# Optimization experiments

Measured on AMD Instinct MI355X. Metric: run time of the kernel, lower is better.

The kernel has to match this reference:

```python
import jax, jax.numpy as jnp
import numpy as np


def silu(x):
    return x * jax.nn.sigmoid(x)


def setup_inputs() -> dict:
    key = jax.random.key(0)
    ks = jax.random.split(key, 12)
    B, S, Dm = 2, 2048, 768
    I, N, R, K = 1536, 16, 48, 4
    s = 0.02
    return {
        "input_states": jax.random.normal(ks[0], (B, S, Dm), jnp.float32),
        "in_proj_w": jax.random.normal(ks[1], (2 * I, Dm), jnp.float32) * s,
        "conv_w": jax.random.normal(ks[2], (I, 1, K), jnp.float32) * s,
        "conv_b": jax.random.normal(ks[3], (I,), jnp.float32) * s,
        "x_proj_w": jax.random.normal(ks[4], (R + 2 * N, I), jnp.float32) * s,
        "dt_proj_w": jax.random.normal(ks[5], (I, R), jnp.float32) * s,
        "dt_proj_b": jax.random.normal(ks[6], (I,), jnp.float32) * s,
        "A_log": jax.random.normal(ks[7], (I, N), jnp.float32) * 0.5,
        "D": jax.random.normal(ks[8], (I,), jnp.float32) * s,
        "out_proj_w": jax.random.normal(ks[9], (Dm, I), jnp.float32) * s,
        "alpha": jax.random.uniform(ks[10], (I,), jnp.float32),
        "feature_gating": jax.random.uniform(ks[11], (I,), jnp.float32),
    }


def reference(input_states, in_proj_w, conv_w, conv_b, x_proj_w,
              dt_proj_w, dt_proj_b, A_log, D, out_proj_w,
              alpha, feature_gating):
    Bsz, S, _ = input_states.shape
    I, N = A_log.shape
    R = dt_proj_w.shape[1]
    K = conv_w.shape[-1]

    # in_proj (no bias), chunk into hidden / gate, each [B, I, S]
    proj = jnp.einsum('bsd,ed->bse', input_states, in_proj_w)  # [B, S, 2I]
    hidden, gate = jnp.split(proj.transpose(0, 2, 1), 2, axis=1)

    # causal depthwise conv1d + SiLU
    h = jax.lax.conv_general_dilated(
        hidden, conv_w, window_strides=(1,), padding=[(K - 1, 0)],
        dimension_numbers=('NCH', 'OIH', 'NCH'), feature_group_count=I)
    h = silu(h + conv_b[None, :, None])  # [B, I, S]

    # x_proj -> time_step, B, C
    ssm_p = jnp.einsum('bis,ei->bse', h, x_proj_w)  # [B, S, R+2N]
    ts, Bm, Cm = jnp.split(ssm_p, [R, R + N], axis=-1)

    dt = jax.nn.softplus(jnp.einsum('bsr,ir->bsi', ts, dt_proj_w) + dt_proj_b)
    dt = dt.transpose(0, 2, 1)                       # [B, I, S]
    dt = dt.at[:, :, -1].multiply(alpha[None, :])    # alpha scales last step

    A = -jnp.exp(A_log.astype(jnp.float32))          # [I, N]
    dA = jnp.exp(A[None, :, None, :] * dt[:, :, :, None])       # [B, I, S, N]
    dBu = dt[:, :, :, None] * Bm[:, None, :, :] * h[:, :, :, None]  # [B, I, S, N]

    def step(state, xs):
        dA_t, dBu_t, C_t = xs
        state = dA_t * state + dBu_t                 # [B, I, N]
        y = jnp.einsum('bin,bn->bi', state, C_t)
        return state, y

    init = jnp.zeros((Bsz, I, N), input_states.dtype)
    _, ys = jax.lax.scan(
        step, init,
        (dA.transpose(2, 0, 1, 3), dBu.transpose(2, 0, 1, 3), Cm.transpose(1, 0, 2)))
    y = ys.transpose(1, 2, 0)                        # [B, I, S]

    y = (y + h * D[None, :, None]) * silu(gate)
    y = y.at[:, :, -1].multiply(feature_gating[None, :])
    return jnp.einsum('bis,di->bsd', y, out_proj_w)  # [B, S, Dm]
```

## Files before the change

kernel.cpp:

```cpp
#include <hip/hip_runtime.h>
#include <math.h>


static constexpr int S_LEN  = 2048;
static constexpr int DMODEL = 768;
static constexpr int ICH    = 1536;
static constexpr int NST    = 16;
static constexpr int MROWS  = 4096;
static constexpr int NCH    = 64;
static constexpr int CHS    = 32;
static constexpr int CSTR   = 2 * ICH * NST;

typedef _Float16 f16;
typedef f16 f16x8 __attribute__((ext_vector_type(8)));
typedef f16 f16x4 __attribute__((ext_vector_type(4)));
typedef f16 f16x2 __attribute__((ext_vector_type(2)));
typedef float f32x4 __attribute__((ext_vector_type(4)));

#if __has_builtin(__builtin_amdgcn_exp2f)
#define EXP2F(x) __builtin_amdgcn_exp2f(x)
#else
#define EXP2F(x) exp2f(x)
#endif

typedef __attribute__((address_space(3))) void lds_void;
typedef const __attribute__((address_space(1))) void glb_void;

__device__ __forceinline__ void glds16(f16* l, const f16* g) {
    __builtin_amdgcn_global_load_lds((glb_void*)g, (lds_void*)l, 16, 0, 0);
}

__device__ __forceinline__ float silu_f(float x) {
    return x / (1.0f + __expf(-x));
}

__global__ __launch_bounds__(256) void cvt3(
    const float* __restrict__ s0, f16* __restrict__ d0, int n0,
    const float* __restrict__ s1, f16* __restrict__ d1, int n1,
    const float* __restrict__ s2, f16* __restrict__ d2)
{
    int i = (blockIdx.x * 256 + threadIdx.x) * 4;
    const float* s; f16* d;
    if (i < n0)            { s = s0 + i;            d = d0 + i; }
    else if (i < n0 + n1)  { s = s1 + (i - n0);     d = d1 + (i - n0); }
    else                   { s = s2 + (i - n0 - n1); d = d2 + (i - n0 - n1); }
    float4 v = *(const float4*)s;
    f16x4 o = { (f16)v.x, (f16)v.y, (f16)v.z, (f16)v.w };
    *(f16x4*)d = o;
}

__global__ __launch_bounds__(256) void k1m(
    const f16* __restrict__ Xh,
    const f16* __restrict__ Wh,
    f16* __restrict__ hidden,
    f16* __restrict__ sgate)
{
    __shared__ __align__(16) f16 As[2][128 * 32];
    __shared__ __align__(16) f16 Bs[2][64 * 32];
    const int tid = threadIdx.x;
    const int lane = tid & 63, wave = tid >> 6;
    const int quad = lane >> 4, l16 = lane & 15;
    const int wm = wave & 1, wn = wave >> 1;
    const int m0 = blockIdx.x * 128, n0 = blockIdx.y * 64;
    const int l_row = lane >> 2, l_c8 = (lane & 3) * 8;

    const f16* Ag = Xh + (size_t)(m0 + wave * 16 + l_row) * 768 + l_c8;
    const f16* Bg = Wh + (size_t)(n0 + wave * 16 + l_row) * 768 + l_c8;
    const int aLo = (wave * 16) * 32, aHi = (64 + wave * 16) * 32;
    const int bOff = (wave * 16) * 32;

#define K1_STAGE(buf, kk)                                        \
    do {                                                         \
        glds16(&As[buf][aLo], Ag + (kk));                        \
        glds16(&As[buf][aHi], Ag + (size_t)64 * 768 + (kk));     \
        glds16(&Bs[buf][bOff], Bg + (kk));                       \
    } while (0)

#define K1_COMPUTE(buf)                                                        \
    do {                                                                       \
        f16x8 af[4], bf[2];                                                    \
        _Pragma("unroll")                                                      \
        for (int mi = 0; mi < 4; ++mi)                                         \
            af[mi] = *(const f16x8*)&As[buf][(wm * 64 + mi * 16 + l16) * 32 + quad * 8]; \
        _Pragma("unroll")                                                      \
        for (int ni = 0; ni < 2; ++ni)                                         \
            bf[ni] = *(const f16x8*)&Bs[buf][(wn * 32 + ni * 16 + l16) * 32 + quad * 8]; \
        _Pragma("unroll")                                                      \
        for (int mi = 0; mi < 4; ++mi)                                         \
            _Pragma("unroll")                                                  \
            for (int ni = 0; ni < 2; ++ni)                                     \
                acc[mi][ni] = __builtin_amdgcn_mfma_f32_16x16x32_f16(          \
                    af[mi], bf[ni], acc[mi][ni], 0, 0, 0);                     \
    } while (0)

    K1_STAGE(0, 0);
    __syncthreads();

    f32x4 acc[4][2] = {};
    for (int k0 = 0; k0 < 768; k0 += 64) {
        K1_STAGE(1, k0 + 32);
        K1_COMPUTE(0);
        __syncthreads();
        if (k0 + 64 < 768) K1_STAGE(0, k0 + 64);
        K1_COMPUTE(1);
        __syncthreads();
    }
#undef K1_STAGE
#undef K1_COMPUTE

    const bool isGate = (n0 >= ICH);
    f16* outp = isGate ? sgate : hidden;
    const int e0 = (isGate ? (n0 - ICH) : n0) + wn * 32 + l16;
    #pragma unroll
    for (int mi = 0; mi < 4; ++mi) {
        #pragma unroll
        for (int ni = 0; ni < 2; ++ni) {
            #pragma unroll
            for (int r = 0; r < 4; ++r) {
                int m = m0 + wm * 64 + mi * 16 + quad * 4 + r;
                int e = e0 + ni * 16;
                float v = acc[mi][ni][r];
                if (isGate) v = silu_f(v);
                outp[(size_t)m * ICH + e] = (f16)v;
            }
        }
    }
}

__global__ __launch_bounds__(256) void k3m(
    const f16* __restrict__ hidden,
    const float* __restrict__ conv_w,
    const float* __restrict__ conv_b,
    const float* __restrict__ xw,
    f16* __restrict__ h,
    float* __restrict__ ssmp)
{
    __shared__ __align__(16) f16 Ah[128 * 32];
    __shared__ __align__(16) f16 Bh[80 * 32];
    __shared__ float4 cwv[96];
    __shared__ float  cbv[96];
    const int tid = threadIdx.x;
    const int lane = tid & 63, wave = tid >> 6;
    const int quad = lane >> 4, l16 = lane & 15;
    const int m0 = blockIdx.x * 128;
    const int kbeg = blockIdx.y * 96;

    if (tid < 96) {
        cwv[tid] = *(const float4*)(conv_w + (size_t)(kbeg + tid) * 4);
        cbv[tid] = conv_b[kbeg + tid];
    }

    f32x4 acc[2][5] = {};
    for (int k0 = kbeg; k0 < kbeg + 96; k0 += 32) {
        __syncthreads();
        #pragma unroll
        for (int it = 0; it < 2; ++it) {
            int slot = tid + it * 256;
            int r_ = slot >> 2, c_ = (slot & 3) * 8;
            int gm = m0 + r_, c = k0 + c_;
            int s = gm & (S_LEN - 1);
            const f16* bp = hidden + (size_t)gm * ICH + c;
            f16x8 x0 = *(const f16x8*)bp;
            f16x8 x1 = *(const f16x8*)(bp - (s >= 1 ? ICH : 0));
            f16x8 x2 = *(const f16x8*)(bp - (s >= 2 ? 2 * ICH : 0));
            f16x8 x3 = *(const f16x8*)(bp - (s >= 3 ? 3 * ICH : 0));
            f16x8 o;
            #pragma unroll
            for (int j = 0; j < 8; ++j) {
                int ci = (k0 - kbeg) + c_ + j;
                float4 w = cwv[ci];
                float v1 = (s >= 1) ? (float)x1[j] : 0.f;
                float v2 = (s >= 2) ? (float)x2[j] : 0.f;
                float v3 = (s >= 3) ? (float)x3[j] : 0.f;
                float r = cbv[ci] + w.x * v3 + w.y * v2 + w.z * v1 + w.w * (float)x0[j];
                o[j] = (f16)silu_f(r);
            }
            *(f16x8*)&Ah[r_ * 32 + c_] = o;
            *(f16x8*)(h + (size_t)gm * ICH + c) = o;
        }
        {
            int c4 = (tid & 7) * 4;
            for (int r = tid >> 3; r < 80; r += 32) {
                float4 v = *(const float4*)(xw + (size_t)r * ICH + k0 + c4);
                f16x4 o = { (f16)v.x, (f16)v.y, (f16)v.z, (f16)v.w };
                *(f16x4*)&Bh[r * 32 + c4] = o;
            }
        }
        __syncthreads();
        f16x8 af[2], bf[5];
        #pragma unroll
        for (int mi = 0; mi < 2; ++mi)
            af[mi] = *(const f16x8*)&Ah[(wave * 32 + mi * 16 + l16) * 32 + quad * 8];
        #pragma unroll
        for (int j = 0; j < 5; ++j)
            bf[j] = *(const f16x8*)&Bh[(j * 16 + l16) * 32 + quad * 8];
        #pragma unroll
        for (int mi = 0; mi < 2; ++mi)
            #pragma unroll
            for (int j = 0; j < 5; ++j)
                acc[mi][j] = __builtin_amdgcn_mfma_f32_16x16x32_f16(
                    af[mi], bf[j], acc[mi][j], 0, 0, 0);
    }
    #pragma unroll
    for (int mi = 0; mi < 2; ++mi) {
        #pragma unroll
        for (int j = 0; j < 5; ++j) {
            #pragma unroll
            for (int r = 0; r < 4; ++r) {
                int m = m0 + wave * 32 + mi * 16 + quad * 4 + r;
                atomicAdd(ssmp + (size_t)m * 80 + j * 16 + l16, acc[mi][j][r]);
            }
        }
    }
}

__global__ __launch_bounds__(256) void k4m(
    const float* __restrict__ ssmp,
    const float* __restrict__ dtw,
    const float* __restrict__ dtb,
    const float* __restrict__ alpha,
    f16* __restrict__ dt)
{
    __shared__ __align__(16) f16 As[128 * 72];
    __shared__ __align__(16) f16 Bs[128 * 72];
    const int tid = threadIdx.x;
    const int lane = tid & 63, wave = tid >> 6;
    const int quad = lane >> 4, l16 = lane & 15;
    const int wm = wave & 1, wn = wave >> 1;
    const int m0 = blockIdx.x * 128, n0 = blockIdx.y * 128;
    const int srow = tid >> 1;
    const int shalf = tid & 1;

    {
        const float* sa = ssmp + (size_t)(m0 + srow) * 80 + shalf * 24;
        const float* sb = dtw + (size_t)(n0 + srow) * 48 + shalf * 24;
        f16* da = &As[srow * 72 + shalf * 24];
        f16* db = &Bs[srow * 72 + shalf * 24];
        #pragma unroll
        for (int j = 0; j < 6; ++j) {
            float4 va = *(const float4*)(sa + 4 * j);
            float4 vb = *(const float4*)(sb + 4 * j);
            f16x4 oa = { (f16)va.x, (f16)va.y, (f16)va.z, (f16)va.w };
            f16x4 ob = { (f16)vb.x, (f16)vb.y, (f16)vb.z, (f16)vb.w };
            *(f16x4*)(da + 4 * j) = oa;
            *(f16x4*)(db + 4 * j) = ob;
        }
        if (shalf) {
            f16x8 z = {};
            *(f16x8*)&As[srow * 72 + 48] = z;
            *(f16x8*)&As[srow * 72 + 56] = z;
            *(f16x8*)&Bs[srow * 72 + 48] = z;
            *(f16x8*)&Bs[srow * 72 + 56] = z;
        }
    }
    __syncthreads();

    f32x4 acc[4][4] = {};
    #pragma unroll
    for (int ks = 0; ks < 2; ++ks) {
        f16x8 af[4], bf[4];
        #pragma unroll
        for (int mi = 0; mi < 4; ++mi)
            af[mi] = *(const f16x8*)&As[(wm * 64 + mi * 16 + l16) * 72 + ks * 32 + quad * 8];
        #pragma unroll
        for (int ni = 0; ni < 4; ++ni)
            bf[ni] = *(const f16x8*)&Bs[(wn * 64 + ni * 16 + l16) * 72 + ks * 32 + quad * 8];
        #pragma unroll
        for (int mi = 0; mi < 4; ++mi)
            #pragma unroll
            for (int ni = 0; ni < 4; ++ni)
                acc[mi][ni] = __builtin_amdgcn_mfma_f32_16x16x32_f16(
                    af[mi], bf[ni], acc[mi][ni], 0, 0, 0);
    }

    #pragma unroll
    for (int ni = 0; ni < 4; ++ni) {
        int e = n0 + wn * 64 + ni * 16 + l16;
        float bias = dtb[e];
        float al = alpha[e];
        #pragma unroll
        for (int mi = 0; mi < 4; ++mi) {
            #pragma unroll
            for (int r = 0; r < 4; ++r) {
                int m = m0 + wm * 64 + mi * 16 + quad * 4 + r;
                float x = acc[mi][ni][r] + bias;
                float sp = (x > 20.0f) ? x : __logf(1.0f + __expf(x));
                if ((m & (S_LEN - 1)) == S_LEN - 1) sp *= al;
                dt[(size_t)m * ICH + e] = (f16)sp;
            }
        }
    }
}

__global__ __launch_bounds__(256) void k5a_chunk(
    const f16* __restrict__ dt,
    const f16* __restrict__ h,
    const float* __restrict__ ssmp,
    const float* __restrict__ A_log,
    float* __restrict__ PArr,
    float* __restrict__ SfArr)
{
    __shared__ float dts[CHS * 64];
    __shared__ float hs[CHS * 64];
    __shared__ float Bc[CHS][16];
    const int tid = threadIdx.x;
    const int n4 = tid & 3;
    const int il = tid >> 2;
    const int i0 = blockIdx.x * 64;
    const int i = i0 + il;
    const int c = blockIdx.y;
    const int b = blockIdx.z;
    const int s0 = c * CHS;
    const size_t row0 = (size_t)(b * S_LEN + s0) * ICH + i0;

    #pragma unroll
    for (int k = 0; k < (CHS * 64) / 512; ++k) {
        int idx = (tid + k * 256) * 2;
        size_t g_off = row0 + (size_t)(idx >> 6) * ICH + (idx & 63);
        f16x2 dv = *(const f16x2*)(dt + g_off);
        f16x2 hv = *(const f16x2*)(h + g_off);
        dts[idx] = (float)dv[0]; dts[idx + 1] = (float)dv[1];
        hs[idx]  = (float)hv[0]; hs[idx + 1]  = (float)hv[1];
    }
    if (tid < CHS * 4) {
        int t = tid >> 2, q = tid & 3;
        *(float4*)&Bc[t][q * 4] =
            *(const float4*)(ssmp + (size_t)(b * S_LEN + s0 + t) * 80 + 48 + q * 4);
    }

    const float L2E = 1.44269504088896f;
    float4 alv = *(const float4*)(A_log + i * NST + n4 * 4);
    float A[4] = { -__expf(alv.x) * L2E, -__expf(alv.y) * L2E,
                   -__expf(alv.z) * L2E, -__expf(alv.w) * L2E };
    float st[4] = {};
    float cdt = 0.f;
    __syncthreads();
    #pragma unroll 4
    for (int t = 0; t < CHS; ++t) {
        float dtv = dts[t * 64 + il];
        float hv  = hs[t * 64 + il];
        float4 Bv = *(const float4*)&Bc[t][n4 * 4];
        cdt += dtv;
        float x = dtv * hv;
        #pragma unroll
        for (int j = 0; j < 4; ++j) {
            float dA = EXP2F(A[j] * dtv);
            st[j] = fmaf(dA, st[j], x * (&Bv.x)[j]);
        }
    }
    size_t base = (size_t)c * CSTR + (size_t)(b * ICH + i) * NST + n4 * 4;
    float4 Pv = { EXP2F(A[0] * cdt), EXP2F(A[1] * cdt),
                  EXP2F(A[2] * cdt), EXP2F(A[3] * cdt) };
    float4 Sv = { st[0], st[1], st[2], st[3] };
    *(float4*)(PArr + base)  = Pv;
    *(float4*)(SfArr + base) = Sv;
}

__global__ __launch_bounds__(256) void k5b_carry(
    const float* PArr,
    const float* __restrict__ SfArr,
    float* CIn)
{
    int idx = blockIdx.x * 256 + threadIdx.x;
    float p[NCH], s[NCH];
    #pragma unroll
    for (int c = 0; c < NCH; ++c) {
        size_t a = (size_t)c * CSTR + idx;
        p[c] = PArr[a];
        s[c] = SfArr[a];
    }
    float carry = 0.f;
    #pragma unroll
    for (int c = 0; c < NCH; ++c) {
        CIn[(size_t)c * CSTR + idx] = carry;
        carry = fmaf(p[c], carry, s[c]);
    }
}

__global__ __launch_bounds__(256) void k5c_emit(
    const f16* __restrict__ dt,
    const f16* __restrict__ h,
    const f16* __restrict__ sgate,
    const float* __restrict__ ssmp,
    const float* __restrict__ A_log,
    const float* __restrict__ Dp,
    const float* __restrict__ fg,
    const float* __restrict__ CIn,
    f16* __restrict__ yh)
{
    __shared__ float dts[CHS * 64];
    __shared__ float hs[CHS * 64];
    __shared__ float gs[CHS * 64];
    __shared__ float BC[CHS][32];
    const int tid = threadIdx.x;
    const int n4 = tid & 3;
    const int il = tid >> 2;
    const int i0 = blockIdx.x * 64;
    const int i = i0 + il;
    const int c = blockIdx.y;
    const int b = blockIdx.z;
    const int s0 = c * CHS;
    const size_t row0 = (size_t)(b * S_LEN + s0) * ICH + i0;

    #pragma unroll
    for (int k = 0; k < (CHS * 64) / 512; ++k) {
        int idx = (tid + k * 256) * 2;
        size_t g_off = row0 + (size_t)(idx >> 6) * ICH + (idx & 63);
        f16x2 dv = *(const f16x2*)(dt + g_off);
        f16x2 v = *(const f16x2*)(h + g_off);
        f16x2 w = *(const f16x2*)(sgate + g_off);
        dts[idx] = (float)dv[0]; dts[idx + 1] = (float)dv[1];
        hs[idx] = (float)v[0]; hs[idx + 1] = (float)v[1];
        gs[idx] = (float)w[0]; gs[idx + 1] = (float)w[1];
    }
    {
        int t = tid >> 3, q = tid & 7;
        *(float4*)&BC[t][q * 4] =
            *(const float4*)(ssmp + (size_t)(b * S_LEN + s0 + t) * 80 + 48 + q * 4);
    }

    const float L2E = 1.44269504088896f;
    float4 alv = *(const float4*)(A_log + i * NST + n4 * 4);
    float A[4] = { -__expf(alv.x) * L2E, -__expf(alv.y) * L2E,
                   -__expf(alv.z) * L2E, -__expf(alv.w) * L2E };
    const float Dv = Dp[i];
    const float fgv = fg[i];
    float4 civ = *(const float4*)(CIn + (size_t)c * CSTR + (size_t)(b * ICH + i) * NST + n4 * 4);
    float st[4] = { civ.x, civ.y, civ.z, civ.w };
    f16* yout = yh + row0 + il;
    const bool last_chunk = (c == NCH - 1);
    __syncthreads();
    #pragma unroll 4
    for (int t = 0; t < CHS; ++t) {
        float dtv = dts[t * 64 + il];
        float hv  = hs[t * 64 + il];
        float4 Bv = *(const float4*)&BC[t][n4 * 4];
        float4 Cv = *(const float4*)&BC[t][16 + n4 * 4];
        float x = dtv * hv;
        float yp = 0.f;
        #pragma unroll
        for (int j = 0; j < 4; ++j) {
            float dA = EXP2F(A[j] * dtv);
            st[j] = fmaf(dA, st[j], x * (&Bv.x)[j]);
            yp = fmaf(st[j], (&Cv.x)[j], yp);
        }
        yp += __shfl_xor(yp, 1, 4);
        yp += __shfl_xor(yp, 2, 4);
        if (n4 == 0) {
            float yv = fmaf(hv, Dv, yp) * gs[t * 64 + il];
            if (last_chunk && t == CHS - 1) yv *= fgv;
            yout[(size_t)t * ICH] = (f16)yv;
        }
    }
}

__global__ __launch_bounds__(256) void k6m(
    const f16* __restrict__ Yh,
    const f16* __restrict__ Wh,
    float* __restrict__ out)
{
    __shared__ __align__(16) f16 As[2][64 * 32];
    __shared__ __align__(16) f16 Bs[2][64 * 32];
    const int tid = threadIdx.x;
    const int lane = tid & 63, wave = tid >> 6;
    const int quad = lane >> 4, l16 = lane & 15;
    const int wm = wave & 1, wn = wave >> 1;
    const int m0 = blockIdx.x * 64, n0 = blockIdx.y * 64;
    const int l_row = lane >> 2, l_c8 = (lane & 3) * 8;

    const f16* Ag = Yh + (size_t)(m0 + wave * 16 + l_row) * ICH + l_c8;
    const f16* Bg = Wh + (size_t)(n0 + wave * 16 + l_row) * ICH + l_c8;
    const int aOff = (wave * 16) * 32;

#define K6_STAGE(buf, kk)                                        \
    do {                                                         \
        glds16(&As[buf][aOff], Ag + (kk));                       \
        glds16(&Bs[buf][aOff], Bg + (kk));                       \
    } while (0)

#define K6_COMPUTE(buf)                                                        \
    do {                                                                       \
        f16x8 af[2], bf[2];                                                    \
        _Pragma("unroll")                                                      \
        for (int mi = 0; mi < 2; ++mi)                                         \
            af[mi] = *(const f16x8*)&As[buf][(wm * 32 + mi * 16 + l16) * 32 + quad * 8]; \
        _Pragma("unroll")                                                      \
        for (int ni = 0; ni < 2; ++ni)                                         \
            bf[ni] = *(const f16x8*)&Bs[buf][(wn * 32 + ni * 16 + l16) * 32 + quad * 8]; \
        _Pragma("unroll")                                                      \
        for (int mi = 0; mi < 2; ++mi)                                         \
            _Pragma("unroll")                                                  \
            for (int ni = 0; ni < 2; ++ni)                                     \
                acc[mi][ni] = __builtin_amdgcn_mfma_f32_16x16x32_f16(          \
                    af[mi], bf[ni], acc[mi][ni], 0, 0, 0);                     \
    } while (0)

    K6_STAGE(0, 0);
    __syncthreads();

    f32x4 acc[2][2] = {};
    for (int k0 = 0; k0 < ICH; k0 += 64) {
        K6_STAGE(1, k0 + 32);
        K6_COMPUTE(0);
        __syncthreads();
        if (k0 + 64 < ICH) K6_STAGE(0, k0 + 64);
        K6_COMPUTE(1);
        __syncthreads();
    }
#undef K6_STAGE
#undef K6_COMPUTE

    #pragma unroll
    for (int mi = 0; mi < 2; ++mi) {
        #pragma unroll
        for (int ni = 0; ni < 2; ++ni) {
            #pragma unroll
            for (int r = 0; r < 4; ++r) {
                int m = m0 + wm * 32 + mi * 16 + quad * 4 + r;
                int d = n0 + wn * 32 + ni * 16 + l16;
                out[(size_t)m * DMODEL + d] = acc[mi][ni][r];
            }
        }
    }
}

extern "C" void kernel_launch(void* const* d_in, const int* in_sizes, int n_in,
                              void* d_out, int out_size, void* d_ws, size_t ws_size,
                              hipStream_t stream) {
    const float* X     = (const float*)d_in[0];
    const float* W1    = (const float*)d_in[1];
    const float* CW    = (const float*)d_in[2];
    const float* CB    = (const float*)d_in[3];
    const float* XW    = (const float*)d_in[4];
    const float* DTW   = (const float*)d_in[5];
    const float* DTB   = (const float*)d_in[6];
    const float* ALOG  = (const float*)d_in[7];
    const float* DD    = (const float*)d_in[8];
    const float* OW    = (const float*)d_in[9];
    const float* ALPHA = (const float*)d_in[10];
    const float* FG    = (const float*)d_in[11];
    float* out = (float*)d_out;

    const size_t NBI = (size_t)MROWS * ICH;
    f16* hidden_h = (f16*)d_ws;
    f16* sgate_h  = hidden_h + NBI;
    f16* h_h      = sgate_h + NBI;
    f16* dt_h     = h_h + NBI;
    float* ssmp   = (float*)(dt_h + NBI);
    f16* Xh       = (f16*)(ssmp + (size_t)MROWS * 80);
    f16* W1h      = Xh + (size_t)MROWS * DMODEL;
    f16* OWh      = W1h + (size_t)2 * ICH * DMODEL;
    float* SfA    = (float*)(OWh + (size_t)DMODEL * ICH);
    float* PArr = (float*)hidden_h;
    float* CIn  = PArr;
    f16* yh     = (f16*)SfA;

    const int nX = MROWS * DMODEL, nW1 = 2 * ICH * DMODEL, nOW = DMODEL * ICH;
    hipMemsetAsync(ssmp, 0, (size_t)MROWS * 80 * sizeof(float), stream);
    cvt3<<<dim3((nX + nW1 + nOW) / 1024), 256, 0, stream>>>(X, Xh, nX, W1, W1h, nW1, OW, OWh);
    k1m<<<dim3(32, 48), 256, 0, stream>>>(Xh, W1h, hidden_h, sgate_h);
    k3m<<<dim3(32, 16), 256, 0, stream>>>(hidden_h, CW, CB, XW, h_h, ssmp);
    k4m<<<dim3(32, 12), 256, 0, stream>>>(ssmp, DTW, DTB, ALPHA, dt_h);
    k5a_chunk<<<dim3(24, NCH, 2), 256, 0, stream>>>(dt_h, h_h, ssmp, ALOG, PArr, SfA);
    k5b_carry<<<dim3(192), 256, 0, stream>>>(PArr, SfA, CIn);
    k5c_emit<<<dim3(24, NCH, 2), 256, 0, stream>>>(dt_h, h_h, sgate_h, ssmp, ALOG, DD, FG, CIn, yh);
    k6m<<<dim3(64, 12), 256, 0, stream>>>(yh, OWh, out);
}
```

Baseline: 243.1 us.

## Widen in_proj GEMM tile, vectorize scan loads, convert out_proj weights in-kernel

The in_proj GEMM tile grows from 128x64 to 128x128, which halves the grid and raises MFMA work per LDS load at the cost of more accumulator registers. The chunked-scan kernels now load dt, h and gate with 16-byte f16x8 accesses instead of f16x2 loops. The out_proj GEMM reads the fp32 weights directly and converts them to f16 in registers before writing LDS, so the separate conversion pass over those weights is dropped. The extra register pressure could lower occupancy, and the weight path no longer uses direct global-to-LDS loads.

```diff
diff --git a/kernel.cpp b/kernel.cpp
--- a/kernel.cpp
+++ b/kernel.cpp
@@ -34,16 +34,14 @@
     return x / (1.0f + __expf(-x));
 }
 
-__global__ __launch_bounds__(256) void cvt3(
+__global__ __launch_bounds__(256) void cvt2(
     const float* __restrict__ s0, f16* __restrict__ d0, int n0,
-    const float* __restrict__ s1, f16* __restrict__ d1, int n1,
-    const float* __restrict__ s2, f16* __restrict__ d2)
+    const float* __restrict__ s1, f16* __restrict__ d1)
 {
     int i = (blockIdx.x * 256 + threadIdx.x) * 4;
     const float* s; f16* d;
-    if (i < n0)            { s = s0 + i;            d = d0 + i; }
-    else if (i < n0 + n1)  { s = s1 + (i - n0);     d = d1 + (i - n0); }
-    else                   { s = s2 + (i - n0 - n1); d = d2 + (i - n0 - n1); }
+    if (i < n0)            { s = s0 + i;        d = d0 + i; }
+    else                   { s = s1 + (i - n0); d = d1 + (i - n0); }
     float4 v = *(const float4*)s;
     f16x4 o = { (f16)v.x, (f16)v.y, (f16)v.z, (f16)v.w };
     *(f16x4*)d = o;
@@ -56,39 +54,39 @@
     f16* __restrict__ sgate)
 {
     __shared__ __align__(16) f16 As[2][128 * 32];
-    __shared__ __align__(16) f16 Bs[2][64 * 32];
+    __shared__ __align__(16) f16 Bs[2][128 * 32];
     const int tid = threadIdx.x;
     const int lane = tid & 63, wave = tid >> 6;
     const int quad = lane >> 4, l16 = lane & 15;
     const int wm = wave & 1, wn = wave >> 1;
-    const int m0 = blockIdx.x * 128, n0 = blockIdx.y * 64;
+    const int m0 = blockIdx.x * 128, n0 = blockIdx.y * 128;
     const int l_row = lane >> 2, l_c8 = (lane & 3) * 8;
 
     const f16* Ag = Xh + (size_t)(m0 + wave * 16 + l_row) * 768 + l_c8;
     const f16* Bg = Wh + (size_t)(n0 + wave * 16 + l_row) * 768 + l_c8;
-    const int aLo = (wave * 16) * 32, aHi = (64 + wave * 16) * 32;
-    const int bOff = (wave * 16) * 32;
+    const int sLo = (wave * 16) * 32, sHi = (64 + wave * 16) * 32;
 
 #define K1_STAGE(buf, kk)                                        \
     do {                                                         \
-        glds16(&As[buf][aLo], Ag + (kk));                        \
-        glds16(&As[buf][aHi], Ag + (size_t)64 * 768 + (kk));     \
-        glds16(&Bs[buf][bOff], Bg + (kk));                       \
+        glds16(&As[buf][sLo], Ag + (kk));                        \
+        glds16(&As[buf][sHi], Ag + (size_t)64 * 768 + (kk));     \
+        glds16(&Bs[buf][sLo], Bg + (kk));                        \
+        glds16(&Bs[buf][sHi], Bg + (size_t)64 * 768 + (kk));     \
     } while (0)
 
 #define K1_COMPUTE(buf)                                                        \
     do {                                                                       \
-        f16x8 af[4], bf[2];                                                    \
+        f16x8 af[4], bf[4];                                                    \
         _Pragma("unroll")                                                      \
         for (int mi = 0; mi < 4; ++mi)                                         \
             af[mi] = *(const f16x8*)&As[buf][(wm * 64 + mi * 16 + l16) * 32 + quad * 8]; \
         _Pragma("unroll")                                                      \
-        for (int ni = 0; ni < 2; ++ni)                                         \
-            bf[ni] = *(const f16x8*)&Bs[buf][(wn * 32 + ni * 16 + l16) * 32 + quad * 8]; \
+        for (int ni = 0; ni < 4; ++ni)                                         \
+            bf[ni] = *(const f16x8*)&Bs[buf][(wn * 64 + ni * 16 + l16) * 32 + quad * 8]; \
         _Pragma("unroll")                                                      \
         for (int mi = 0; mi < 4; ++mi)                                         \
             _Pragma("unroll")                                                  \
-            for (int ni = 0; ni < 2; ++ni)                                     \
+            for (int ni = 0; ni < 4; ++ni)                                     \
                 acc[mi][ni] = __builtin_amdgcn_mfma_f32_16x16x32_f16(          \
                     af[mi], bf[ni], acc[mi][ni], 0, 0, 0);                     \
     } while (0)
@@ -96,7 +94,7 @@
     K1_STAGE(0, 0);
     __syncthreads();
 
-    f32x4 acc[4][2] = {};
+    f32x4 acc[4][4] = {};
     for (int k0 = 0; k0 < 768; k0 += 64) {
         K1_STAGE(1, k0 + 32);
         K1_COMPUTE(0);
@@ -110,11 +108,11 @@
 
     const bool isGate = (n0 >= ICH);
     f16* outp = isGate ? sgate : hidden;
-    const int e0 = (isGate ? (n0 - ICH) : n0) + wn * 32 + l16;
+    const int e0 = (isGate ? (n0 - ICH) : n0) + wn * 64 + l16;
     #pragma unroll
     for (int mi = 0; mi < 4; ++mi) {
         #pragma unroll
-        for (int ni = 0; ni < 2; ++ni) {
+        for (int ni = 0; ni < 4; ++ni) {
             #pragma unroll
             for (int r = 0; r < 4; ++r) {
                 int m = m0 + wm * 64 + mi * 16 + quad * 4 + r;
@@ -313,14 +311,16 @@
     const int s0 = c * CHS;
     const size_t row0 = (size_t)(b * S_LEN + s0) * ICH + i0;
 
-    #pragma unroll
-    for (int k = 0; k < (CHS * 64) / 512; ++k) {
-        int idx = (tid + k * 256) * 2;
-        size_t g_off = row0 + (size_t)(idx >> 6) * ICH + (idx & 63);
-        f16x2 dv = *(const f16x2*)(dt + g_off);
-        f16x2 hv = *(const f16x2*)(h + g_off);
-        dts[idx] = (float)dv[0]; dts[idx + 1] = (float)dv[1];
-        hs[idx]  = (float)hv[0]; hs[idx + 1]  = (float)hv[1];
+    {
+        int r = tid >> 3, c8 = (tid & 7) * 8;
+        size_t g_off = row0 + (size_t)r * ICH + c8;
+        f16x8 dv = *(const f16x8*)(dt + g_off);
+        f16x8 hv = *(const f16x8*)(h + g_off);
+        #pragma unroll
+        for (int j = 0; j < 8; ++j) {
+            dts[r * 64 + c8 + j] = (float)dv[j];
+            hs[r * 64 + c8 + j]  = (float)hv[j];
+        }
     }
     if (tid < CHS * 4) {
         int t = tid >> 2, q = tid & 3;
@@ -402,16 +402,18 @@
     const int s0 = c * CHS;
     const size_t row0 = (size_t)(b * S_LEN + s0) * ICH + i0;
 
-    #pragma unroll
-    for (int k = 0; k < (CHS * 64) / 512; ++k) {
-        int idx = (tid + k * 256) * 2;
-        size_t g_off = row0 + (size_t)(idx >> 6) * ICH + (idx & 63);
-        f16x2 dv = *(const f16x2*)(dt + g_off);
-        f16x2 v = *(const f16x2*)(h + g_off);
-        f16x2 w = *(const f16x2*)(sgate + g_off);
-        dts[idx] = (float)dv[0]; dts[idx + 1] = (float)dv[1];
-        hs[idx] = (float)v[0]; hs[idx + 1] = (float)v[1];
-        gs[idx] = (float)w[0]; gs[idx + 1] = (float)w[1];
+    {
+        int r = tid >> 3, c8 = (tid & 7) * 8;
+        size_t g_off = row0 + (size_t)r * ICH + c8;
+        f16x8 dv = *(const f16x8*)(dt + g_off);
+        f16x8 hv = *(const f16x8*)(h + g_off);
+        f16x8 gv = *(const f16x8*)(sgate + g_off);
+        #pragma unroll
+        for (int j = 0; j < 8; ++j) {
+            dts[r * 64 + c8 + j] = (float)dv[j];
+            hs[r * 64 + c8 + j]  = (float)hv[j];
+            gs[r * 64 + c8 + j]  = (float)gv[j];
+        }
     }
     {
         int t = tid >> 3, q = tid & 7;
@@ -456,7 +458,7 @@
 
 __global__ __launch_bounds__(256) void k6m(
     const f16* __restrict__ Yh,
-    const f16* __restrict__ Wh,
+    const float* __restrict__ OWf,
     float* __restrict__ out)
 {
     __shared__ __align__(16) f16 As[2][64 * 32];
@@ -469,13 +471,24 @@
     const int l_row = lane >> 2, l_c8 = (lane & 3) * 8;
 
     const f16* Ag = Yh + (size_t)(m0 + wave * 16 + l_row) * ICH + l_c8;
-    const f16* Bg = Wh + (size_t)(n0 + wave * 16 + l_row) * ICH + l_c8;
     const int aOff = (wave * 16) * 32;
-
-#define K6_STAGE(buf, kk)                                        \
+    const int brow = tid >> 2, bc8 = (tid & 3) * 8;
+    const float* Bgf = OWf + (size_t)(n0 + brow) * ICH + bc8;
+    float4 vb0, vb1;
+
+#define K6_STAGEA(buf, kk) glds16(&As[buf][aOff], Ag + (kk))
+
+#define K6_LOADB(kk)                                             \
     do {                                                         \
-        glds16(&As[buf][aOff], Ag + (kk));                       \
-        glds16(&Bs[buf][aOff], Bg + (kk));                       \
+        vb0 = *(const float4*)(Bgf + (kk));                      \
+        vb1 = *(const float4*)(Bgf + (kk) + 4);                  \
+    } while (0)
+
+#define K6_WRITEB(buf)                                                         \
+    do {                                                                       \
+        f16x8 o = { (f16)vb0.x, (f16)vb0.y, (f16)vb0.z, (f16)vb0.w,            \
+                    (f16)vb1.x, (f16)vb1.y, (f16)vb1.z, (f16)vb1.w };          \
+        *(f16x8*)&Bs[buf][brow * 32 + bc8] = o;                                \
     } while (0)
 
 #define K6_COMPUTE(buf)                                                        \
@@ -495,19 +508,29 @@
                     af[mi], bf[ni], acc[mi][ni], 0, 0, 0);                     \
     } while (0)
 
-    K6_STAGE(0, 0);
+    K6_STAGEA(0, 0);
+    K6_LOADB(0);
+    K6_WRITEB(0);
     __syncthreads();
 
     f32x4 acc[2][2] = {};
     for (int k0 = 0; k0 < ICH; k0 += 64) {
-        K6_STAGE(1, k0 + 32);
+        K6_STAGEA(1, k0 + 32);
+        K6_LOADB(k0 + 32);
         K6_COMPUTE(0);
+        K6_WRITEB(1);
         __syncthreads();
-        if (k0 + 64 < ICH) K6_STAGE(0, k0 + 64);
+        if (k0 + 64 < ICH) {
+            K6_STAGEA(0, k0 + 64);
+            K6_LOADB(k0 + 64);
+        }
         K6_COMPUTE(1);
+        if (k0 + 64 < ICH) K6_WRITEB(0);
         __syncthreads();
     }
-#undef K6_STAGE
+#undef K6_STAGEA
+#undef K6_LOADB
+#undef K6_WRITEB
 #undef K6_COMPUTE
 
     #pragma unroll
@@ -549,20 +572,19 @@
     float* ssmp   = (float*)(dt_h + NBI);
     f16* Xh       = (f16*)(ssmp + (size_t)MROWS * 80);
     f16* W1h      = Xh + (size_t)MROWS * DMODEL;
-    f16* OWh      = W1h + (size_t)2 * ICH * DMODEL;
-    float* SfA    = (float*)(OWh + (size_t)DMODEL * ICH);
+    float* SfA    = (float*)(W1h + (size_t)2 * ICH * DMODEL);
     float* PArr = (float*)hidden_h;
     float* CIn  = PArr;
     f16* yh     = (f16*)SfA;
 
-    const int nX = MROWS * DMODEL, nW1 = 2 * ICH * DMODEL, nOW = DMODEL * ICH;
+    const int nX = MROWS * DMODEL, nW1 = 2 * ICH * DMODEL;
     hipMemsetAsync(ssmp, 0, (size_t)MROWS * 80 * sizeof(float), stream);
-    cvt3<<<dim3((nX + nW1 + nOW) / 1024), 256, 0, stream>>>(X, Xh, nX, W1, W1h, nW1, OW, OWh);
-    k1m<<<dim3(32, 48), 256, 0, stream>>>(Xh, W1h, hidden_h, sgate_h);
+    cvt2<<<dim3((nX + nW1) / 1024), 256, 0, stream>>>(X, Xh, nX, W1, W1h);
+    k1m<<<dim3(32, 24), 256, 0, stream>>>(Xh, W1h, hidden_h, sgate_h);
     k3m<<<dim3(32, 16), 256, 0, stream>>>(hidden_h, CW, CB, XW, h_h, ssmp);
     k4m<<<dim3(32, 12), 256, 0, stream>>>(ssmp, DTW, DTB, ALPHA, dt_h);
     k5a_chunk<<<dim3(24, NCH, 2), 256, 0, stream>>>(dt_h, h_h, ssmp, ALOG, PArr, SfA);
     k5b_carry<<<dim3(192), 256, 0, stream>>>(PArr, SfA, CIn);
     k5c_emit<<<dim3(24, NCH, 2), 256, 0, stream>>>(dt_h, h_h, sgate_h, ssmp, ALOG, DD, FG, CIn, yh);
-    k6m<<<dim3(64, 12), 256, 0, stream>>>(yh, OWh, out);
-}
+    k6m<<<dim3(64, 12), 256, 0, stream>>>(yh, OW, out);
+}
```

After: 242.9 us. Within noise of the previous version (-0.1%).
